# Kernel tuning notes

Hardware: AMD Instinct MI355X
Metric: run time of the kernel (lower is better)

## Reference

```python
import jax, jax.numpy as jnp
import numpy as np


def setup_inputs() -> dict:
    key = jax.random.key(0)
    k1, k2, k3, k4, k5 = jax.random.split(key, 5)
    B, S, D_IN, D_OUT = 4, 2048, 4096, 4096
    x = jax.random.normal(k1, (B, S, D_IN), dtype=jnp.float32)
    q_weight = jax.random.randint(k2, (D_OUT, D_IN), 0, 256, dtype=jnp.int32)
    scale = jax.random.uniform(k3, (), dtype=jnp.float32) * 0.01 + 1e-4
    zero_point = jnp.round(jax.random.uniform(k4, (), dtype=jnp.float32) * 255.0)
    bias = jax.random.normal(k5, (D_OUT,), dtype=jnp.float32)
    return {"x": x, "q_weight": q_weight, "scale": scale,
            "zero_point": zero_point, "bias": bias}


def reference(x, q_weight, scale, zero_point, bias):
    # Dequantize: w = scale * (q - zero_point), per-tensor scalar scale/zp.
    weight = scale * (q_weight.astype(jnp.float32) - zero_point)  # [out, in]
    # F.linear: y = x @ w.T + b
    return jnp.einsum('bsi,oi->bso', x, weight) + bias
```

## Files before the change

kernel.cpp:

```cpp
#include <hip/hip_runtime.h>
#include <hip/hip_bf16.h>


typedef __attribute__((ext_vector_type(8))) __bf16 bf16x8;
typedef __attribute__((ext_vector_type(4))) float f32x4;
typedef __attribute__((ext_vector_type(4))) int i32x4;
typedef __attribute__((ext_vector_type(8))) unsigned short u16x8;

#define M_DIM 8192
#define N_DIM 4096
#define K_DIM 4096
#define BM 256
#define BN 256
#define BK 64
#define NT (K_DIM / BK)

#define MFMA16(A, B, C) __builtin_amdgcn_mfma_f32_16x16x32_bf16(A, B, C, 0, 0, 0)

__device__ __forceinline__ unsigned short f2bf(float f) {
  __hip_bfloat16 h = __float2bfloat16(f);
  unsigned short u;
  __builtin_memcpy(&u, &h, 2);
  return u;
}

__global__ __launch_bounds__(256) void cvt_x_kernel(const float* __restrict__ x,
                                                    unsigned short* __restrict__ out) {
  size_t i = (size_t)blockIdx.x * 256 + threadIdx.x;
  f32x4 a = ((const f32x4*)x)[2 * i];
  f32x4 b = ((const f32x4*)x)[2 * i + 1];
  u16x8 o;
  o[0] = f2bf(a[0]); o[1] = f2bf(a[1]); o[2] = f2bf(a[2]); o[3] = f2bf(a[3]);
  o[4] = f2bf(b[0]); o[5] = f2bf(b[1]); o[6] = f2bf(b[2]); o[7] = f2bf(b[3]);
  *(u16x8*)(out + 8 * i) = o;
}

__global__ __launch_bounds__(256) void cvt_w_kernel(const int* __restrict__ q,
                                                    const float* __restrict__ zp_ptr,
                                                    unsigned short* __restrict__ out) {
  const float zp = *zp_ptr;
  size_t i = (size_t)blockIdx.x * 256 + threadIdx.x;
  i32x4 a = ((const i32x4*)q)[2 * i];
  i32x4 b = ((const i32x4*)q)[2 * i + 1];
  u16x8 o;
  o[0] = f2bf((float)a[0] - zp); o[1] = f2bf((float)a[1] - zp);
  o[2] = f2bf((float)a[2] - zp); o[3] = f2bf((float)a[3] - zp);
  o[4] = f2bf((float)b[0] - zp); o[5] = f2bf((float)b[1] - zp);
  o[6] = f2bf((float)b[2] - zp); o[7] = f2bf((float)b[3] - zp);
  *(u16x8*)(out + 8 * i) = o;
}

__device__ __forceinline__ void stage2(const char* s0, const char* s1, char* ldsT,
                                       int h, int Ti, int chunk0, int chunk1) {
  const size_t off = (size_t)Ti * 128 + (size_t)h * 1048576;
  __builtin_amdgcn_global_load_lds(
      (const __attribute__((address_space(1))) void*)(s0 + off),
      (__attribute__((address_space(3))) void*)(ldsT + h * 16384 + chunk0), 16, 0, 0);
  __builtin_amdgcn_global_load_lds(
      (const __attribute__((address_space(1))) void*)(s1 + off),
      (__attribute__((address_space(3))) void*)(ldsT + h * 16384 + chunk1), 16, 0, 0);
}

__device__ __forceinline__ void ktile(
    int T, const char* pak0, const char* pak1, const char* pbk0, const char* pbk1,
    char* curA, char* curB, char* nxtA,
    const char* srcA0, const char* srcA1, const char* srcB0, const char* srcB1,
    int chunk0, int chunk1, f32x4 (&acc)[8][4]) {
  bf16x8 af[4][2], b0f[2][2], b1f[2][2];

#pragma unroll
  for (int fi = 0; fi < 4; ++fi) {
    af[fi][0] = *(const bf16x8*)(pak0 + fi * 2048);
    af[fi][1] = *(const bf16x8*)(pak1 + fi * 2048);
  }
#pragma unroll
  for (int fj = 0; fj < 2; ++fj) {
    b0f[fj][0] = *(const bf16x8*)(pbk0 + fj * 2048);
    b0f[fj][1] = *(const bf16x8*)(pbk1 + fj * 2048);
    b1f[fj][0] = *(const bf16x8*)(pbk0 + 4096 + fj * 2048);
    b1f[fj][1] = *(const bf16x8*)(pbk1 + 4096 + fj * 2048);
  }
  if (T < NT - 1) stage2(srcA0, srcA1, nxtA, 1, T + 1, chunk0, chunk1);
  asm volatile("s_waitcnt lgkmcnt(0)" ::: "memory");
  __builtin_amdgcn_s_barrier();
  __builtin_amdgcn_s_setprio(1);
#pragma unroll
  for (int fi = 0; fi < 4; ++fi)
#pragma unroll
    for (int fj = 0; fj < 2; ++fj) {
      acc[fi][fj] = MFMA16(af[fi][0], b0f[fj][0], acc[fi][fj]);
      acc[fi][fj] = MFMA16(af[fi][1], b0f[fj][1], acc[fi][fj]);
    }
#pragma unroll
  for (int fi = 0; fi < 4; ++fi)
#pragma unroll
    for (int fj = 0; fj < 2; ++fj) {
      acc[fi][2 + fj] = MFMA16(af[fi][0], b1f[fj][0], acc[fi][2 + fj]);
      acc[fi][2 + fj] = MFMA16(af[fi][1], b1f[fj][1], acc[fi][2 + fj]);
    }
  __builtin_amdgcn_s_setprio(0);

#pragma unroll
  for (int fi = 0; fi < 4; ++fi) {
    af[fi][0] = *(const bf16x8*)(pak0 + 8192 + fi * 2048);
    af[fi][1] = *(const bf16x8*)(pak1 + 8192 + fi * 2048);
  }
  if (T < NT - 2) {
    stage2(srcB0, srcB1, curB, 0, T + 2, chunk0, chunk1);
    stage2(srcB0, srcB1, curB, 1, T + 2, chunk0, chunk1);
    stage2(srcA0, srcA1, curA, 0, T + 2, chunk0, chunk1);
  }
  if (T < NT - 2) asm volatile("s_waitcnt vmcnt(6)" ::: "memory");
  else            asm volatile("s_waitcnt vmcnt(0)" ::: "memory");
  asm volatile("s_waitcnt lgkmcnt(0)" ::: "memory");
  __builtin_amdgcn_s_barrier();
  __builtin_amdgcn_s_setprio(1);
#pragma unroll
  for (int fi = 0; fi < 4; ++fi)
#pragma unroll
    for (int fj = 0; fj < 2; ++fj) {
      acc[4 + fi][2 + fj] = MFMA16(af[fi][0], b1f[fj][0], acc[4 + fi][2 + fj]);
      acc[4 + fi][2 + fj] = MFMA16(af[fi][1], b1f[fj][1], acc[4 + fi][2 + fj]);
    }
#pragma unroll
  for (int fi = 0; fi < 4; ++fi)
#pragma unroll
    for (int fj = 0; fj < 2; ++fj) {
      acc[4 + fi][fj] = MFMA16(af[fi][0], b0f[fj][0], acc[4 + fi][fj]);
      acc[4 + fi][fj] = MFMA16(af[fi][1], b0f[fj][1], acc[4 + fi][fj]);
    }
  __builtin_amdgcn_s_setprio(0);
}

__global__ __launch_bounds__(512, 2) void gemm8_kernel(
    const unsigned short* __restrict__ A, const unsigned short* __restrict__ B,
    const float* __restrict__ scale_ptr, const float* __restrict__ bias,
    float* __restrict__ C) {
  __shared__ __align__(16) char lds[131072];

  const int t = threadIdx.x;
  const int lane = t & 63;
  const int w = t >> 6;
  const int wm = w >> 2;
  const int wn = w & 3;
  const int ll = lane & 15;
  const int lh = lane >> 4;

  const int nwg = gridDim.x * gridDim.y;
  const int flat = blockIdx.y * gridDim.x + blockIdx.x;
  const int per = nwg >> 3;
  const int sw = (flat & 7) * per + (flat >> 3);
  const int tn = sw & (N_DIM / BN - 1);
  const int tm = sw / (N_DIM / BN);
  const size_t gm0 = (size_t)tm * BM;
  const size_t gn0 = (size_t)tn * BN;

  char* lA0 = (char*)lds;
  char* lB0 = (char*)lds + 32768;
  char* lA1 = (char*)lds + 65536;
  char* lB1 = (char*)lds + 98304;

  const int sbase = (lh * 16) ^ ((ll & 7) << 4);
  const char* pa0k0 = lA0 + wm * 16384 + ll * 128 + sbase;
  const char* pa0k1 = lA0 + wm * 16384 + ll * 128 + (sbase ^ 64);
  const char* pb0k0 = lB0 + wn * 8192 + ll * 128 + sbase;
  const char* pb0k1 = lB0 + wn * 8192 + ll * 128 + (sbase ^ 64);
  const char* pa1k0 = pa0k0 + 65536;
  const char* pa1k1 = pa0k1 + 65536;
  const char* pb1k0 = pb0k0 + 65536;
  const char* pb1k1 = pb0k1 + 65536;

  const int rowS0 = w * 16 + (lane >> 3);
  const int rowS1 = w * 16 + 8 + (lane >> 3);
  const int colSB = ((lane & 7) * 16) ^ (((lane >> 3) & 7) << 4);
  const int chunk0 = w * 2048;
  const int chunk1 = w * 2048 + 1024;
  const char* srcA0 = (const char*)A + (gm0 + rowS0) * (size_t)(K_DIM * 2) + colSB;
  const char* srcA1 = (const char*)A + (gm0 + rowS1) * (size_t)(K_DIM * 2) + colSB;
  const char* srcB0 = (const char*)B + (gn0 + rowS0) * (size_t)(K_DIM * 2) + colSB;
  const char* srcB1 = (const char*)B + (gn0 + rowS1) * (size_t)(K_DIM * 2) + colSB;

  f32x4 acc[8][4] = {};

  stage2(srcA0, srcA1, lA0, 0, 0, chunk0, chunk1);
  stage2(srcA0, srcA1, lA0, 1, 0, chunk0, chunk1);
  stage2(srcB0, srcB1, lB0, 0, 0, chunk0, chunk1);
  stage2(srcB0, srcB1, lB0, 1, 0, chunk0, chunk1);
  stage2(srcB0, srcB1, lB1, 0, 1, chunk0, chunk1);
  stage2(srcB0, srcB1, lB1, 1, 1, chunk0, chunk1);
  stage2(srcA0, srcA1, lA1, 0, 1, chunk0, chunk1);
  asm volatile("s_waitcnt vmcnt(6)" ::: "memory");
  __builtin_amdgcn_s_barrier();

  for (int T2 = 0; T2 < NT; T2 += 2) {
    ktile(T2, pa0k0, pa0k1, pb0k0, pb0k1, lA0, lB0, lA1,
          srcA0, srcA1, srcB0, srcB1, chunk0, chunk1, acc);
    ktile(T2 + 1, pa1k0, pa1k1, pb1k0, pb1k1, lA1, lB1, lA0,
          srcA0, srcA1, srcB0, srcB1, chunk0, chunk1, acc);
  }

  const float sc = *scale_ptr;
#pragma unroll
  for (int nh = 0; nh < 2; ++nh)
#pragma unroll
    for (int fj = 0; fj < 2; ++fj) {
      const size_t col = gn0 + wn * 64 + nh * 32 + fj * 16 + ll;
      const float bv = bias[col];
#pragma unroll
      for (int mh = 0; mh < 2; ++mh)
#pragma unroll
        for (int fi = 0; fi < 4; ++fi) {
          const size_t row0 = gm0 + wm * 128 + mh * 64 + fi * 16 + lh * 4;
          const f32x4 v = acc[mh * 4 + fi][nh * 2 + fj];
#pragma unroll
          for (int r = 0; r < 4; ++r)
            C[(row0 + r) * N_DIM + col] = sc * v[r] + bv;
        }
    }
}

__global__ __launch_bounds__(256, 2) void gemm_fallback_kernel(
    const float* __restrict__ Aptr, const int* __restrict__ Wptr,
    const float* __restrict__ scale_ptr, const float* __restrict__ zp_ptr,
    const float* __restrict__ bias, float* __restrict__ C) {
  __shared__ unsigned short As[128 * 32];
  __shared__ unsigned short Ws[128 * 32];
  const int t = threadIdx.x;
  const int lane = t & 63;
  const int w = t >> 6;
  const int wm = w >> 1, wn = w & 1;
  const size_t gm0 = (size_t)blockIdx.y * 128;
  const size_t gn0 = (size_t)blockIdx.x * 128;
  f32x4 acc[4][4] = {};
  const float zp = *zp_ptr;
  for (int k0 = 0; k0 < K_DIM; k0 += 32) {
    __syncthreads();
    const int row = t >> 1;
    const int kh = (t & 1) * 16;
    const float* sa = Aptr + (gm0 + row) * (size_t)K_DIM + k0 + kh;
    f32x4 a0 = ((const f32x4*)sa)[0], a1 = ((const f32x4*)sa)[1];
    f32x4 a2 = ((const f32x4*)sa)[2], a3 = ((const f32x4*)sa)[3];
    u16x8 o0, o1;
    o0[0] = f2bf(a0[0]); o0[1] = f2bf(a0[1]); o0[2] = f2bf(a0[2]); o0[3] = f2bf(a0[3]);
    o0[4] = f2bf(a1[0]); o0[5] = f2bf(a1[1]); o0[6] = f2bf(a1[2]); o0[7] = f2bf(a1[3]);
    o1[0] = f2bf(a2[0]); o1[1] = f2bf(a2[1]); o1[2] = f2bf(a2[2]); o1[3] = f2bf(a2[3]);
    o1[4] = f2bf(a3[0]); o1[5] = f2bf(a3[1]); o1[6] = f2bf(a3[2]); o1[7] = f2bf(a3[3]);
    *(u16x8*)&As[row * 32 + kh] = o0;
    *(u16x8*)&As[row * 32 + kh + 8] = o1;
    const int* sw = Wptr + (gn0 + row) * (size_t)K_DIM + k0 + kh;
    i32x4 w0 = ((const i32x4*)sw)[0], w1 = ((const i32x4*)sw)[1];
    i32x4 w2 = ((const i32x4*)sw)[2], w3 = ((const i32x4*)sw)[3];
    u16x8 p0, p1;
    p0[0] = f2bf((float)w0[0] - zp); p0[1] = f2bf((float)w0[1] - zp);
    p0[2] = f2bf((float)w0[2] - zp); p0[3] = f2bf((float)w0[3] - zp);
    p0[4] = f2bf((float)w1[0] - zp); p0[5] = f2bf((float)w1[1] - zp);
    p0[6] = f2bf((float)w1[2] - zp); p0[7] = f2bf((float)w1[3] - zp);
    p1[0] = f2bf((float)w2[0] - zp); p1[1] = f2bf((float)w2[1] - zp);
    p1[2] = f2bf((float)w2[2] - zp); p1[3] = f2bf((float)w2[3] - zp);
    p1[4] = f2bf((float)w3[0] - zp); p1[5] = f2bf((float)w3[1] - zp);
    p1[6] = f2bf((float)w3[2] - zp); p1[7] = f2bf((float)w3[3] - zp);
    *(u16x8*)&Ws[row * 32 + kh] = p0;
    *(u16x8*)&Ws[row * 32 + kh + 8] = p1;
    __syncthreads();
    bf16x8 af[4], bfr[4];
#pragma unroll
    for (int f = 0; f < 4; ++f) {
      af[f] = *(const bf16x8*)&As[(wm * 64 + f * 16 + (lane & 15)) * 32 + (lane >> 4) * 8];
      bfr[f] = *(const bf16x8*)&Ws[(wn * 64 + f * 16 + (lane & 15)) * 32 + (lane >> 4) * 8];
    }
#pragma unroll
    for (int i = 0; i < 4; ++i)
#pragma unroll
      for (int j = 0; j < 4; ++j)
        acc[i][j] = MFMA16(af[i], bfr[j], acc[i][j]);
  }
  const float sc = *scale_ptr;
#pragma unroll
  for (int i = 0; i < 4; ++i) {
    const int rbase = wm * 64 + i * 16 + ((lane >> 4) << 2);
#pragma unroll
    for (int j = 0; j < 4; ++j) {
      const size_t col = gn0 + wn * 64 + j * 16 + (lane & 15);
      const float bv = bias[col];
#pragma unroll
      for (int r = 0; r < 4; ++r)
        C[(gm0 + rbase + r) * N_DIM + col] = sc * acc[i][j][r] + bv;
    }
  }
}

extern "C" void kernel_launch(void* const* d_in, const int* in_sizes, int n_in,
                              void* d_out, int out_size, void* d_ws, size_t ws_size,
                              hipStream_t stream) {
  const float* x = (const float*)d_in[0];
  const int* q = (const int*)d_in[1];
  const float* scale = (const float*)d_in[2];
  const float* zp = (const float*)d_in[3];
  const float* bias = (const float*)d_in[4];
  float* out = (float*)d_out;

  const size_t needA = (size_t)M_DIM * K_DIM * 2;
  const size_t needW = (size_t)N_DIM * K_DIM * 2;

  if (ws_size >= needA + needW) {
    unsigned short* Abf = (unsigned short*)d_ws;
    unsigned short* Wbf = (unsigned short*)((char*)d_ws + needA);
    cvt_x_kernel<<<(M_DIM * (size_t)K_DIM) / (8 * 256), 256, 0, stream>>>(x, Abf);
    cvt_w_kernel<<<(N_DIM * (size_t)K_DIM) / (8 * 256), 256, 0, stream>>>(q, zp, Wbf);
    dim3 grid(N_DIM / BN, M_DIM / BM);
    gemm8_kernel<<<grid, 512, 0, stream>>>(Abf, Wbf, scale, bias, out);
  } else {
    dim3 grid(N_DIM / 128, M_DIM / 128);
    gemm_fallback_kernel<<<grid, 256, 0, stream>>>(x, q, scale, zp, bias, out);
  }
}
```

Before: 279.0 us.

## Triple-buffer A tiles and double-buffer B to need one barrier per k-tile

Restructures the LDS pipeline so A uses three buffers and B two, with B for the next tile and A two tiles ahead issued during the current tile's MFMAs. This cuts the two barriers and lgkmcnt waits per k-tile down to one vmcnt wait plus one barrier. It also drops the setprio hints and interleaves the MFMA loops. The main loop becomes a 6-tile unrolled cycle with a 4-tile tail. LDS grows from 128KB to 160KB, which uses the full per-CU LDS and removes any slack for co-resident blocks.

```diff
diff --git a/kernel.cpp b/kernel.cpp
--- a/kernel.cpp
+++ b/kernel.cpp
@@ -62,81 +62,67 @@
 }
 
 __device__ __forceinline__ void ktile(
-    int T, const char* pak0, const char* pak1, const char* pbk0, const char* pbk1,
-    char* curA, char* curB, char* nxtA,
+    int T,
+    const char* paK0, const char* paK1, const char* pbK0, const char* pbK1,
+    char* stA, char* stB,
     const char* srcA0, const char* srcA1, const char* srcB0, const char* srcB1,
     int chunk0, int chunk1, f32x4 (&acc)[8][4]) {
   bf16x8 af[4][2], b0f[2][2], b1f[2][2];
 
 #pragma unroll
   for (int fi = 0; fi < 4; ++fi) {
-    af[fi][0] = *(const bf16x8*)(pak0 + fi * 2048);
-    af[fi][1] = *(const bf16x8*)(pak1 + fi * 2048);
+    af[fi][0] = *(const bf16x8*)(paK0 + fi * 2048);
+    af[fi][1] = *(const bf16x8*)(paK1 + fi * 2048);
   }
 #pragma unroll
   for (int fj = 0; fj < 2; ++fj) {
-    b0f[fj][0] = *(const bf16x8*)(pbk0 + fj * 2048);
-    b0f[fj][1] = *(const bf16x8*)(pbk1 + fj * 2048);
-    b1f[fj][0] = *(const bf16x8*)(pbk0 + 4096 + fj * 2048);
-    b1f[fj][1] = *(const bf16x8*)(pbk1 + 4096 + fj * 2048);
-  }
-  if (T < NT - 1) stage2(srcA0, srcA1, nxtA, 1, T + 1, chunk0, chunk1);
-  asm volatile("s_waitcnt lgkmcnt(0)" ::: "memory");
-  __builtin_amdgcn_s_barrier();
-  __builtin_amdgcn_s_setprio(1);
+    b0f[fj][0] = *(const bf16x8*)(pbK0 + fj * 2048);
+    b0f[fj][1] = *(const bf16x8*)(pbK1 + fj * 2048);
+    b1f[fj][0] = *(const bf16x8*)(pbK0 + 4096 + fj * 2048);
+    b1f[fj][1] = *(const bf16x8*)(pbK1 + 4096 + fj * 2048);
+  }
+  if (T < NT - 1) {
+    stage2(srcB0, srcB1, stB, 0, T + 1, chunk0, chunk1);
+    stage2(srcB0, srcB1, stB, 1, T + 1, chunk0, chunk1);
+  }
 #pragma unroll
   for (int fi = 0; fi < 4; ++fi)
 #pragma unroll
     for (int fj = 0; fj < 2; ++fj) {
-      acc[fi][fj] = MFMA16(af[fi][0], b0f[fj][0], acc[fi][fj]);
-      acc[fi][fj] = MFMA16(af[fi][1], b0f[fj][1], acc[fi][fj]);
-    }
-#pragma unroll
-  for (int fi = 0; fi < 4; ++fi)
-#pragma unroll
-    for (int fj = 0; fj < 2; ++fj) {
+      acc[fi][fj]     = MFMA16(af[fi][0], b0f[fj][0], acc[fi][fj]);
+      acc[fi][fj]     = MFMA16(af[fi][1], b0f[fj][1], acc[fi][fj]);
       acc[fi][2 + fj] = MFMA16(af[fi][0], b1f[fj][0], acc[fi][2 + fj]);
       acc[fi][2 + fj] = MFMA16(af[fi][1], b1f[fj][1], acc[fi][2 + fj]);
     }
-  __builtin_amdgcn_s_setprio(0);
-
 #pragma unroll
   for (int fi = 0; fi < 4; ++fi) {
-    af[fi][0] = *(const bf16x8*)(pak0 + 8192 + fi * 2048);
-    af[fi][1] = *(const bf16x8*)(pak1 + 8192 + fi * 2048);
+    af[fi][0] = *(const bf16x8*)(paK0 + 8192 + fi * 2048);
+    af[fi][1] = *(const bf16x8*)(paK1 + 8192 + fi * 2048);
   }
   if (T < NT - 2) {
-    stage2(srcB0, srcB1, curB, 0, T + 2, chunk0, chunk1);
-    stage2(srcB0, srcB1, curB, 1, T + 2, chunk0, chunk1);
-    stage2(srcA0, srcA1, curA, 0, T + 2, chunk0, chunk1);
-  }
-  if (T < NT - 2) asm volatile("s_waitcnt vmcnt(6)" ::: "memory");
-  else            asm volatile("s_waitcnt vmcnt(0)" ::: "memory");
-  asm volatile("s_waitcnt lgkmcnt(0)" ::: "memory");
-  __builtin_amdgcn_s_barrier();
-  __builtin_amdgcn_s_setprio(1);
+    stage2(srcA0, srcA1, stA, 0, T + 2, chunk0, chunk1);
+    stage2(srcA0, srcA1, stA, 1, T + 2, chunk0, chunk1);
+  }
 #pragma unroll
   for (int fi = 0; fi < 4; ++fi)
 #pragma unroll
     for (int fj = 0; fj < 2; ++fj) {
       acc[4 + fi][2 + fj] = MFMA16(af[fi][0], b1f[fj][0], acc[4 + fi][2 + fj]);
       acc[4 + fi][2 + fj] = MFMA16(af[fi][1], b1f[fj][1], acc[4 + fi][2 + fj]);
-    }
-#pragma unroll
-  for (int fi = 0; fi < 4; ++fi)
-#pragma unroll
-    for (int fj = 0; fj < 2; ++fj) {
-      acc[4 + fi][fj] = MFMA16(af[fi][0], b0f[fj][0], acc[4 + fi][fj]);
-      acc[4 + fi][fj] = MFMA16(af[fi][1], b0f[fj][1], acc[4 + fi][fj]);
-    }
-  __builtin_amdgcn_s_setprio(0);
+      acc[4 + fi][fj]     = MFMA16(af[fi][0], b0f[fj][0], acc[4 + fi][fj]);
+      acc[4 + fi][fj]     = MFMA16(af[fi][1], b0f[fj][1], acc[4 + fi][fj]);
+    }
+  if (T < NT - 2) asm volatile("s_waitcnt vmcnt(4)" ::: "memory");
+  else            asm volatile("s_waitcnt vmcnt(0)" ::: "memory");
+  __builtin_amdgcn_s_barrier();
+  asm volatile("" ::: "memory");
 }
 
 __global__ __launch_bounds__(512, 2) void gemm8_kernel(
     const unsigned short* __restrict__ A, const unsigned short* __restrict__ B,
     const float* __restrict__ scale_ptr, const float* __restrict__ bias,
     float* __restrict__ C) {
-  __shared__ __align__(16) char lds[131072];
+  __shared__ __align__(16) char lds[163840];
 
   const int t = threadIdx.x;
   const int lane = t & 63;
@@ -156,19 +142,19 @@
   const size_t gn0 = (size_t)tn * BN;
 
   char* lA0 = (char*)lds;
-  char* lB0 = (char*)lds + 32768;
-  char* lA1 = (char*)lds + 65536;
-  char* lB1 = (char*)lds + 98304;
+  char* lA1 = (char*)lds + 32768;
+  char* lA2 = (char*)lds + 65536;
+  char* lB0 = (char*)lds + 98304;
+  char* lB1 = (char*)lds + 131072;
 
   const int sbase = (lh * 16) ^ ((ll & 7) << 4);
-  const char* pa0k0 = lA0 + wm * 16384 + ll * 128 + sbase;
-  const char* pa0k1 = lA0 + wm * 16384 + ll * 128 + (sbase ^ 64);
-  const char* pb0k0 = lB0 + wn * 8192 + ll * 128 + sbase;
-  const char* pb0k1 = lB0 + wn * 8192 + ll * 128 + (sbase ^ 64);
-  const char* pa1k0 = pa0k0 + 65536;
-  const char* pa1k1 = pa0k1 + 65536;
-  const char* pb1k0 = pb0k0 + 65536;
-  const char* pb1k1 = pb0k1 + 65536;
+  const int aoff = wm * 16384 + ll * 128;
+  const int boff = wn * 8192 + ll * 128;
+  const char* pA0k0 = lA0 + aoff + sbase;       const char* pA0k1 = lA0 + aoff + (sbase ^ 64);
+  const char* pA1k0 = lA1 + aoff + sbase;       const char* pA1k1 = lA1 + aoff + (sbase ^ 64);
+  const char* pA2k0 = lA2 + aoff + sbase;       const char* pA2k1 = lA2 + aoff + (sbase ^ 64);
+  const char* pB0k0 = lB0 + boff + sbase;       const char* pB0k1 = lB0 + boff + (sbase ^ 64);
+  const char* pB1k0 = lB1 + boff + sbase;       const char* pB1k1 = lB1 + boff + (sbase ^ 64);
 
   const int rowS0 = w * 16 + (lane >> 3);
   const int rowS1 = w * 16 + 8 + (lane >> 3);
@@ -186,18 +172,24 @@
   stage2(srcA0, srcA1, lA0, 1, 0, chunk0, chunk1);
   stage2(srcB0, srcB1, lB0, 0, 0, chunk0, chunk1);
   stage2(srcB0, srcB1, lB0, 1, 0, chunk0, chunk1);
-  stage2(srcB0, srcB1, lB1, 0, 1, chunk0, chunk1);
-  stage2(srcB0, srcB1, lB1, 1, 1, chunk0, chunk1);
   stage2(srcA0, srcA1, lA1, 0, 1, chunk0, chunk1);
-  asm volatile("s_waitcnt vmcnt(6)" ::: "memory");
+  stage2(srcA0, srcA1, lA1, 1, 1, chunk0, chunk1);
+  asm volatile("s_waitcnt vmcnt(4)" ::: "memory");
   __builtin_amdgcn_s_barrier();
-
-  for (int T2 = 0; T2 < NT; T2 += 2) {
-    ktile(T2, pa0k0, pa0k1, pb0k0, pb0k1, lA0, lB0, lA1,
-          srcA0, srcA1, srcB0, srcB1, chunk0, chunk1, acc);
-    ktile(T2 + 1, pa1k0, pa1k1, pb1k0, pb1k1, lA1, lB1, lA0,
-          srcA0, srcA1, srcB0, srcB1, chunk0, chunk1, acc);
-  }
+  asm volatile("" ::: "memory");
+
+  for (int T6 = 0; T6 < NT - 4; T6 += 6) {
+    ktile(T6 + 0, pA0k0, pA0k1, pB0k0, pB0k1, lA2, lB1, srcA0, srcA1, srcB0, srcB1, chunk0, chunk1, acc);
+    ktile(T6 + 1, pA1k0, pA1k1, pB1k0, pB1k1, lA0, lB0, srcA0, srcA1, srcB0, srcB1, chunk0, chunk1, acc);
+    ktile(T6 + 2, pA2k0, pA2k1, pB0k0, pB0k1, lA1, lB1, srcA0, srcA1, srcB0, srcB1, chunk0, chunk1, acc);
+    ktile(T6 + 3, pA0k0, pA0k1, pB1k0, pB1k1, lA2, lB0, srcA0, srcA1, srcB0, srcB1, chunk0, chunk1, acc);
+    ktile(T6 + 4, pA1k0, pA1k1, pB0k0, pB0k1, lA0, lB1, srcA0, srcA1, srcB0, srcB1, chunk0, chunk1, acc);
+    ktile(T6 + 5, pA2k0, pA2k1, pB1k0, pB1k1, lA1, lB0, srcA0, srcA1, srcB0, srcB1, chunk0, chunk1, acc);
+  }
+  ktile(NT - 4, pA0k0, pA0k1, pB0k0, pB0k1, lA2, lB1, srcA0, srcA1, srcB0, srcB1, chunk0, chunk1, acc);
+  ktile(NT - 3, pA1k0, pA1k1, pB1k0, pB1k1, lA0, lB0, srcA0, srcA1, srcB0, srcB1, chunk0, chunk1, acc);
+  ktile(NT - 2, pA2k0, pA2k1, pB0k0, pB0k1, lA1, lB1, srcA0, srcA1, srcB0, srcB1, chunk0, chunk1, acc);
+  ktile(NT - 1, pA0k0, pA0k1, pB1k0, pB1k1, lA2, lB0, srcA0, srcA1, srcB0, srcB1, chunk0, chunk1, acc);
 
   const float sc = *scale_ptr;
 #pragma unroll
```

Measured after the change: 304.0 us. 9.0% more time.
